# Optimization experiments

Hardware: AMD Instinct MI355X
Metric: run time of the kernel (lower is better)

Reference implementation:

```python
import jax, jax.numpy as jnp
import numpy as np

N = 50000       # num_entities / nodes
E = 100000      # edges
K = 8           # incoming edge-graph neighbors per edge
D_NODE = 64
D_EDGE = 64
H = 4
DH = D_EDGE // H
DIN = D_EDGE + 2 * D_NODE  # [edge_feat, node_feat[src], node_feat[dst]]


def setup_inputs() -> dict:
    key = jax.random.key(0)
    ks = jax.random.split(key, 6)
    node_features = jax.random.normal(ks[0], (N, D_NODE), jnp.float32)
    edge_features = jax.random.normal(ks[1], (E, D_EDGE), jnp.float32)
    edge_index = jax.random.randint(ks[2], (2, E), 0, N)
    node_tiers = jax.random.randint(ks[3], (N,), 0, 4, dtype=jnp.int32)
    # edge adjacency (line graph): each edge attends to K other edges
    adj_dst = jnp.repeat(jnp.arange(E), K)                       # [A]
    adj_src = jax.random.randint(ks[4], (E * K,), 0, E)          # [A]
    # learned params: two EdgeAttention layers, each Wq/Wk/Wv [DIN,D_EDGE], Wo [D_EDGE,D_EDGE]
    wkeys = jax.random.split(ks[5], 8)
    def w(k, fan_in, fan_out):
        return jax.random.normal(k, (fan_in, fan_out), jnp.float32) * np.float32(1.0 / np.sqrt(fan_in))
    params = {}
    for li in (1, 2):
        base = (li - 1) * 4
        params[f'l{li}_Wq'] = w(wkeys[base + 0], DIN, D_EDGE)
        params[f'l{li}_Wk'] = w(wkeys[base + 1], DIN, D_EDGE)
        params[f'l{li}_Wv'] = w(wkeys[base + 2], DIN, D_EDGE)
        params[f'l{li}_Wo'] = w(wkeys[base + 3], D_EDGE, D_EDGE)
    return dict(node_features=node_features, edge_features=edge_features,
                edge_index=edge_index, node_tiers=node_tiers,
                adj_src=adj_src, adj_dst=adj_dst, **params)


def _edge_attention(node_f, edge_f, edge_index, adj_src, adj_dst, Wq, Wk, Wv, Wo):
    # x: edge feature conditioned on endpoint node features  [E, DIN]
    x = jnp.concatenate([edge_f, node_f[edge_index[0]], node_f[edge_index[1]]], axis=-1)
    q = (x @ Wq).reshape(E, H, DH)
    k = (x @ Wk).reshape(E, H, DH)
    v = (x @ Wv).reshape(E, H, DH)
    scale = np.float32(1.0 / np.sqrt(DH))
    # scores per adjacency pair  [A, H]
    s = jnp.einsum('ahd,ahd->ah', q[adj_dst], k[adj_src]) * scale
    # segment softmax over incoming neighbors of each dst edge
    m = jax.ops.segment_max(s, adj_dst, num_segments=E)          # [E, H]
    e = jnp.exp(s - m[adj_dst])                                   # [A, H]
    denom = jax.ops.segment_sum(e, adj_dst, num_segments=E)      # [E, H]
    alpha = e / denom[adj_dst]                                    # [A, H]
    out = jax.ops.segment_sum(alpha[..., None] * v[adj_src], adj_dst, num_segments=E)  # [E,H,DH]
    return edge_f + out.reshape(E, D_EDGE) @ Wo                   # residual


def reference(node_features, edge_features, edge_index, node_tiers, adj_src, adj_dst,
              l1_Wq, l1_Wk, l1_Wv, l1_Wo, l2_Wq, l2_Wk, l2_Wv, l2_Wo):
    ef = _edge_attention(node_features, edge_features, edge_index, adj_src, adj_dst,
                         l1_Wq, l1_Wk, l1_Wv, l1_Wo)
    ef = _edge_attention(node_features, ef, edge_index, adj_src, adj_dst,
                         l2_Wq, l2_Wk, l2_Wv, l2_Wo)
    return ef  # updated edge features of the output DeltaGraph
```

## Files before the change

kernel.cpp:

```cpp
#include <hip/hip_runtime.h>

#define NE 100000
#define NN 50000

typedef short short8 __attribute__((ext_vector_type(8)));
typedef float f32x4 __attribute__((ext_vector_type(4)));
typedef unsigned short ushort;
typedef unsigned int uint;

__device__ inline ushort f2bf(float f) {
    unsigned int u = __float_as_uint(f);
    u += 0x7FFFu + ((u >> 16) & 1u);
    return (ushort)(u >> 16);
}
__device__ inline float bf2f(ushort u) {
    return __uint_as_float((unsigned int)u << 16);
}

__device__ inline short8 pack_bf8(float4 a, float4 b) {
    short8 r;
    r[0] = (short)f2bf(a.x); r[1] = (short)f2bf(a.y);
    r[2] = (short)f2bf(a.z); r[3] = (short)f2bf(a.w);
    r[4] = (short)f2bf(b.x); r[5] = (short)f2bf(b.y);
    r[6] = (short)f2bf(b.z); r[7] = (short)f2bf(b.w);
    return r;
}

__device__ inline void pack_qkv_slot(int slot, const float* Wq, const float* Wk,
                                     const float* Wv, ushort* wf)
{
    int lane = slot & 63;
    int st = slot >> 6;
    int s = st / 12, t = st % 12;
    int n = t * 16 + (lane & 15);
    int kb = s * 32 + (lane >> 4) * 8;
    const float* w = (n < 64) ? Wq : (n < 128) ? Wk : Wv;
    int nn = n & 63;
    #pragma unroll
    for (int j = 0; j < 8; ++j)
        wf[(size_t)slot * 8 + j] = f2bf(w[(size_t)(kb + j) * 64 + nn]);
}

__device__ inline void pack_wo_slot(int slot, const float* Wo, ushort* wf)
{
    int lane = slot & 63;
    int st = slot >> 6;
    int s = st / 4, t = st % 4;
    int n = t * 16 + (lane & 15);
    int kb = s * 32 + (lane >> 4) * 8;
    #pragma unroll
    for (int j = 0; j < 8; ++j)
        wf[(size_t)slot * 8 + j] = f2bf(Wo[(size_t)(kb + j) * 64 + n]);
}

__global__ __launch_bounds__(256) void prep_all(
    const float* __restrict__ l1Wq, const float* __restrict__ l1Wk,
    const float* __restrict__ l1Wv, const float* __restrict__ l1Wo,
    const float* __restrict__ l2Wq, const float* __restrict__ l2Wk,
    const float* __restrict__ l2Wv, const float* __restrict__ l2Wo,
    ushort* __restrict__ wf1, ushort* __restrict__ wf2,
    ushort* __restrict__ wo1, ushort* __restrict__ wo2)
{
    int idx = blockIdx.x * 256 + threadIdx.x;
    if (idx < 4608)            pack_qkv_slot(idx,         l1Wq, l1Wk, l1Wv, wf1);
    else if (idx < 9216)       pack_qkv_slot(idx - 4608,  l2Wq, l2Wk, l2Wv, wf2);
    else if (idx < 9728)       pack_wo_slot (idx - 9216,  l1Wo, wo1);
    else if (idx < 10240)      pack_wo_slot (idx - 9728,  l2Wo, wo2);
}

#define MFMA_B16(a, b, c) c = __builtin_amdgcn_mfma_f32_16x16x32_bf16(a, b, c, 0, 0, 0)

#define GLP const __attribute__((address_space(1))) uint*
#define LDP __attribute__((address_space(3))) uint*

#define STAGE(ph) do {                                                         \
    const char* gs_ = (const char*)wfrag + (size_t)(ph) * 24576 + (size_t)l * 16; \
    __builtin_amdgcn_global_load_lds((GLP)(gs_ + (size_t)(w*6+0)*1024), (LDP)(ldsb + (size_t)(w*6+0)*1024), 16, 0, 0); \
    __builtin_amdgcn_global_load_lds((GLP)(gs_ + (size_t)(w*6+1)*1024), (LDP)(ldsb + (size_t)(w*6+1)*1024), 16, 0, 0); \
    __builtin_amdgcn_global_load_lds((GLP)(gs_ + (size_t)(w*6+2)*1024), (LDP)(ldsb + (size_t)(w*6+2)*1024), 16, 0, 0); \
    __builtin_amdgcn_global_load_lds((GLP)(gs_ + (size_t)(w*6+3)*1024), (LDP)(ldsb + (size_t)(w*6+3)*1024), 16, 0, 0); \
    __builtin_amdgcn_global_load_lds((GLP)(gs_ + (size_t)(w*6+4)*1024), (LDP)(ldsb + (size_t)(w*6+4)*1024), 16, 0, 0); \
    __builtin_amdgcn_global_load_lds((GLP)(gs_ + (size_t)(w*6+5)*1024), (LDP)(ldsb + (size_t)(w*6+5)*1024), 16, 0, 0); \
} while (0)

#define KSTEP(Areg, si) do {                                                   \
    const char* lb_ = ldsb + (size_t)(si) * 12288 + (size_t)l * 16;            \
    short8 b0_  = *(const short8*)(lb_ + 0);                                   \
    short8 b1_  = *(const short8*)(lb_ + 1024);                                \
    short8 b2_  = *(const short8*)(lb_ + 2048);                                \
    short8 b3_  = *(const short8*)(lb_ + 3072);                                \
    short8 b4_  = *(const short8*)(lb_ + 4096);                                \
    short8 b5_  = *(const short8*)(lb_ + 5120);                                \
    short8 b6_  = *(const short8*)(lb_ + 6144);                                \
    short8 b7_  = *(const short8*)(lb_ + 7168);                                \
    short8 b8_  = *(const short8*)(lb_ + 8192);                                \
    short8 b9_  = *(const short8*)(lb_ + 9216);                                \
    short8 b10_ = *(const short8*)(lb_ + 10240);                               \
    short8 b11_ = *(const short8*)(lb_ + 11264);                               \
    MFMA_B16(Areg, b0_,  c0);  MFMA_B16(Areg, b1_,  c1);                       \
    MFMA_B16(Areg, b2_,  c2);  MFMA_B16(Areg, b3_,  c3);                       \
    MFMA_B16(Areg, b4_,  c4);  MFMA_B16(Areg, b5_,  c5);                       \
    MFMA_B16(Areg, b6_,  c6);  MFMA_B16(Areg, b7_,  c7);                       \
    MFMA_B16(Areg, b8_,  c8);  MFMA_B16(Areg, b9_,  c9);                       \
    MFMA_B16(Areg, b10_, c10); MFMA_B16(Areg, b11_, c11);                      \
} while (0)

#define STORE_T(creg, dstp, cloc) do {                                         \
    ushort* dp_ = (dstp) + (cloc);                                             \
    int row_ = e0 + kg * 4;                                                    \
    if (row_ + 0 < NE) dp_[(size_t)(row_ + 0) * 64] = f2bf(creg[0]);           \
    if (row_ + 1 < NE) dp_[(size_t)(row_ + 1) * 64] = f2bf(creg[1]);           \
    if (row_ + 2 < NE) dp_[(size_t)(row_ + 2) * 64] = f2bf(creg[2]);           \
    if (row_ + 3 < NE) dp_[(size_t)(row_ + 3) * 64] = f2bf(creg[3]);           \
} while (0)

__global__ __launch_bounds__(256) void qkv_mfma(
    const float* __restrict__ ef, const float* __restrict__ nodef,
    const int* __restrict__ eidx, const ushort* __restrict__ wfrag,
    ushort* __restrict__ qo, ushort* __restrict__ ko, ushort* __restrict__ vo)
{
    __shared__ __align__(1024) char ldsb[24 * 1024];

    const int tid = threadIdx.x;
    const int l   = tid & 63;
    const int w   = tid >> 6;
    const int r   = l & 15;
    const int kg  = l >> 4;
    const int e0  = blockIdx.x * 64 + w * 16;
    const int e   = e0 + r;
    const int ec  = (e < NE) ? e : NE - 1;

    STAGE(0);

    const int koff = kg * 8;
    const float* rp0 = ef    + (size_t)ec * 64;
    const float* rp1 = nodef + (size_t)eidx[ec] * 64;
    const float* rp2 = nodef + (size_t)eidx[NE + ec] * 64;

    short8 A0 = pack_bf8(*(const float4*)(rp0 + koff),      *(const float4*)(rp0 + koff + 4));
    short8 A1 = pack_bf8(*(const float4*)(rp0 + 32 + koff), *(const float4*)(rp0 + 36 + koff));
    short8 A2 = pack_bf8(*(const float4*)(rp1 + koff),      *(const float4*)(rp1 + koff + 4));
    short8 A3 = pack_bf8(*(const float4*)(rp1 + 32 + koff), *(const float4*)(rp1 + 36 + koff));
    short8 A4 = pack_bf8(*(const float4*)(rp2 + koff),      *(const float4*)(rp2 + koff + 4));
    short8 A5 = pack_bf8(*(const float4*)(rp2 + 32 + koff), *(const float4*)(rp2 + 36 + koff));

    f32x4 c0 = (f32x4)(0.f), c1 = (f32x4)(0.f), c2  = (f32x4)(0.f), c3  = (f32x4)(0.f);
    f32x4 c4 = (f32x4)(0.f), c5 = (f32x4)(0.f), c6  = (f32x4)(0.f), c7  = (f32x4)(0.f);
    f32x4 c8 = (f32x4)(0.f), c9 = (f32x4)(0.f), c10 = (f32x4)(0.f), c11 = (f32x4)(0.f);

    __syncthreads();
    KSTEP(A0, 0);
    KSTEP(A1, 1);
    __syncthreads();
    STAGE(1);
    __syncthreads();
    KSTEP(A2, 0);
    KSTEP(A3, 1);
    __syncthreads();
    STAGE(2);
    __syncthreads();
    KSTEP(A4, 0);
    KSTEP(A5, 1);

    STORE_T(c0,  qo, 0 * 16 + r);
    STORE_T(c1,  qo, 1 * 16 + r);
    STORE_T(c2,  qo, 2 * 16 + r);
    STORE_T(c3,  qo, 3 * 16 + r);
    STORE_T(c4,  ko, 0 * 16 + r);
    STORE_T(c5,  ko, 1 * 16 + r);
    STORE_T(c6,  ko, 2 * 16 + r);
    STORE_T(c7,  ko, 3 * 16 + r);
    STORE_T(c8,  vo, 0 * 16 + r);
    STORE_T(c9,  vo, 1 * 16 + r);
    STORE_T(c10, vo, 2 * 16 + r);
    STORE_T(c11, vo, 3 * 16 + r);
}

__global__ __launch_bounds__(256) void attn_kernel(
    const ushort* __restrict__ q, const ushort* __restrict__ kbuf,
    const ushort* __restrict__ vbuf, const int* __restrict__ adj_src,
    ushort* __restrict__ ao)
{
    const int wid  = (blockIdx.x * 256 + threadIdx.x) >> 6;
    const int lane = threadIdx.x & 63;
    if (wid >= NE) return;
    const int e    = wid;
    const int half = lane >> 5;
    const int l32  = lane & 31;

    const int4 nb = *(const int4*)(adj_src + e * 8 + half * 4);
    const int nbr0 = nb.x, nbr1 = nb.y, nbr2 = nb.z, nbr3 = nb.w;

    ushort2 qu = *(const ushort2*)(q + (size_t)e * 64 + l32 * 2);
    const float q0 = bf2f(qu.x), q1 = bf2f(qu.y);

    ushort2 ku0 = *(const ushort2*)(kbuf + (size_t)nbr0 * 64 + l32 * 2);
    ushort2 ku1 = *(const ushort2*)(kbuf + (size_t)nbr1 * 64 + l32 * 2);
    ushort2 ku2 = *(const ushort2*)(kbuf + (size_t)nbr2 * 64 + l32 * 2);
    ushort2 ku3 = *(const ushort2*)(kbuf + (size_t)nbr3 * 64 + l32 * 2);
    ushort2 vu0 = *(const ushort2*)(vbuf + (size_t)nbr0 * 64 + l32 * 2);
    ushort2 vu1 = *(const ushort2*)(vbuf + (size_t)nbr1 * 64 + l32 * 2);
    ushort2 vu2 = *(const ushort2*)(vbuf + (size_t)nbr2 * 64 + l32 * 2);
    ushort2 vu3 = *(const ushort2*)(vbuf + (size_t)nbr3 * 64 + l32 * 2);

    float s0 = q0 * bf2f(ku0.x) + q1 * bf2f(ku0.y);
    float s1 = q0 * bf2f(ku1.x) + q1 * bf2f(ku1.y);
    float s2 = q0 * bf2f(ku2.x) + q1 * bf2f(ku2.y);
    float s3 = q0 * bf2f(ku3.x) + q1 * bf2f(ku3.y);
    s0 += __shfl_xor(s0, 1); s0 += __shfl_xor(s0, 2); s0 += __shfl_xor(s0, 4);
    s1 += __shfl_xor(s1, 1); s1 += __shfl_xor(s1, 2); s1 += __shfl_xor(s1, 4);
    s2 += __shfl_xor(s2, 1); s2 += __shfl_xor(s2, 2); s2 += __shfl_xor(s2, 4);
    s3 += __shfl_xor(s3, 1); s3 += __shfl_xor(s3, 2); s3 += __shfl_xor(s3, 4);
    s0 *= 0.25f; s1 *= 0.25f; s2 *= 0.25f; s3 *= 0.25f;

    float m = fmaxf(fmaxf(s0, s1), fmaxf(s2, s3));
    m = fmaxf(m, __shfl_xor(m, 32));
    float w0 = __expf(s0 - m), w1 = __expf(s1 - m);
    float w2 = __expf(s2 - m), w3 = __expf(s3 - m);
    float den = w0 + w1 + w2 + w3;
    den += __shfl_xor(den, 32);
    const float inv = 1.f / den;

    float ox = 0.f, oy = 0.f;
    ox = fmaf(w0, bf2f(vu0.x), ox); oy = fmaf(w0, bf2f(vu0.y), oy);
    ox = fmaf(w1, bf2f(vu1.x), ox); oy = fmaf(w1, bf2f(vu1.y), oy);
    ox = fmaf(w2, bf2f(vu2.x), ox); oy = fmaf(w2, bf2f(vu2.y), oy);
    ox = fmaf(w3, bf2f(vu3.x), ox); oy = fmaf(w3, bf2f(vu3.y), oy);
    ox = (ox + __shfl_xor(ox, 32)) * inv;
    oy = (oy + __shfl_xor(oy, 32)) * inv;

    if (lane < 32) {
        ushort2 o;
        o.x = f2bf(ox);
        o.y = f2bf(oy);
        *(ushort2*)(ao + (size_t)e * 64 + l32 * 2) = o;
    }
}

__global__ __launch_bounds__(256) void wo_mfma(
    const float* __restrict__ ef_in, const ushort* __restrict__ attn,
    const ushort* __restrict__ wofrag, float* __restrict__ efo)
{
    const int wave = threadIdx.x >> 6;
    const int lane = threadIdx.x & 63;
    const int r  = lane & 15;
    const int kg = lane >> 4;
    const int e0 = blockIdx.x * 64 + wave * 16;
    const int e  = e0 + r;
    const int ec = (e < NE) ? e : NE - 1;

    short8 af0 = *(const short8*)(attn + (size_t)ec * 64 + kg * 8);
    short8 af1 = *(const short8*)(attn + (size_t)ec * 64 + 32 + kg * 8);

    const char* wf = (const char*)wofrag + (size_t)lane * 16;
    f32x4 d0 = (f32x4)(0.f), d1 = (f32x4)(0.f), d2 = (f32x4)(0.f), d3 = (f32x4)(0.f);
    short8 g0 = *(const short8*)(wf + 0 * 1024);
    short8 g1 = *(const short8*)(wf + 1 * 1024);
    short8 g2 = *(const short8*)(wf + 2 * 1024);
    short8 g3 = *(const short8*)(wf + 3 * 1024);
    MFMA_B16(af0, g0, d0); MFMA_B16(af0, g1, d1);
    MFMA_B16(af0, g2, d2); MFMA_B16(af0, g3, d3);
    g0 = *(const short8*)(wf + 4 * 1024);
    g1 = *(const short8*)(wf + 5 * 1024);
    g2 = *(const short8*)(wf + 6 * 1024);
    g3 = *(const short8*)(wf + 7 * 1024);
    MFMA_B16(af1, g0, d0); MFMA_B16(af1, g1, d1);
    MFMA_B16(af1, g2, d2); MFMA_B16(af1, g3, d3);

    const int orow = e0 + kg * 4;
    #pragma unroll
    for (int t = 0; t < 4; ++t) {
        const f32x4 dd = (t == 0) ? d0 : (t == 1) ? d1 : (t == 2) ? d2 : d3;
        const int c = t * 16 + r;
        #pragma unroll
        for (int j = 0; j < 4; ++j) {
            int row = orow + j;
            if (row < NE) {
                size_t off = (size_t)row * 64 + c;
                efo[off] = dd[j] + ef_in[off];
            }
        }
    }
}

extern "C" void kernel_launch(void* const* d_in, const int* in_sizes, int n_in,
                              void* d_out, int out_size, void* d_ws, size_t ws_size,
                              hipStream_t stream)
{
    const float* nodef   = (const float*)d_in[0];
    const float* ef      = (const float*)d_in[1];
    const int*   eidx    = (const int*)d_in[2];
    const int*   adj_src = (const int*)d_in[4];
    const float* l1Wq = (const float*)d_in[6];
    const float* l1Wk = (const float*)d_in[7];
    const float* l1Wv = (const float*)d_in[8];
    const float* l1Wo = (const float*)d_in[9];
    const float* l2Wq = (const float*)d_in[10];
    const float* l2Wk = (const float*)d_in[11];
    const float* l2Wv = (const float*)d_in[12];
    const float* l2Wo = (const float*)d_in[13];

    ushort* q  = (ushort*)d_ws;
    ushort* k  = q  + (size_t)NE * 64;
    ushort* v  = k  + (size_t)NE * 64;
    ushort* ao = v  + (size_t)NE * 64;
    ushort* wf1 = ao + (size_t)NE * 64;
    ushort* wf2 = wf1 + 36864;
    ushort* wo1 = wf2 + 36864;
    ushort* wo2 = wo1 + 4096;
    float* out = (float*)d_out;

    dim3 blk(256);
    const int gq = (NE + 63) / 64;
    const int ga = (NE + 3) / 4;
    const int gw = (NE + 63) / 64;

    prep_all<<<40, blk, 0, stream>>>(l1Wq, l1Wk, l1Wv, l1Wo,
                                     l2Wq, l2Wk, l2Wv, l2Wo,
                                     wf1, wf2, wo1, wo2);

    qkv_mfma<<<gq, blk, 0, stream>>>(ef, nodef, eidx, wf1, q, k, v);
    attn_kernel<<<ga, blk, 0, stream>>>(q, k, v, adj_src, ao);
    wo_mfma<<<gw, blk, 0, stream>>>(ef, ao, wo1, out);
    qkv_mfma<<<gq, blk, 0, stream>>>(out, nodef, eidx, wf2, q, k, v);
    attn_kernel<<<ga, blk, 0, stream>>>(q, k, v, adj_src, ao);
    wo_mfma<<<gw, blk, 0, stream>>>(out, ao, wo2, out);
}
```

Measured before the change: 149.2 us.

## Restructure QKV GEMM: per-wave output-column split, direct B loads, LDS-staged coalesced stores

The QKV projection kernel now gives each block 32 edges. Each wave computes 3 of the 12 output column tiles for both 16-row groups, reading weight fragments straight from global/L2 instead of staging all weights into LDS with barriers between phases. Results are transposed through a small LDS buffer and written as coalesced 16-byte rows for q, k and v, replacing the scattered 2-byte strided stores. The trade is more redundant A-row gathers per edge across waves and more weight traffic per block, in exchange for no phase barriers, smaller LDS, and much better store coalescing.

```diff
diff --git a/kernel.cpp b/kernel.cpp
--- a/kernel.cpp
+++ b/kernel.cpp
@@ -70,110 +70,95 @@
 
 #define MFMA_B16(a, b, c) c = __builtin_amdgcn_mfma_f32_16x16x32_bf16(a, b, c, 0, 0, 0)
 
-#define GLP const __attribute__((address_space(1))) uint*
-#define LDP __attribute__((address_space(3))) uint*
-
-#define STAGE(ph) do {                                                         \
-    const char* gs_ = (const char*)wfrag + (size_t)(ph) * 24576 + (size_t)l * 16; \
-    __builtin_amdgcn_global_load_lds((GLP)(gs_ + (size_t)(w*6+0)*1024), (LDP)(ldsb + (size_t)(w*6+0)*1024), 16, 0, 0); \
-    __builtin_amdgcn_global_load_lds((GLP)(gs_ + (size_t)(w*6+1)*1024), (LDP)(ldsb + (size_t)(w*6+1)*1024), 16, 0, 0); \
-    __builtin_amdgcn_global_load_lds((GLP)(gs_ + (size_t)(w*6+2)*1024), (LDP)(ldsb + (size_t)(w*6+2)*1024), 16, 0, 0); \
-    __builtin_amdgcn_global_load_lds((GLP)(gs_ + (size_t)(w*6+3)*1024), (LDP)(ldsb + (size_t)(w*6+3)*1024), 16, 0, 0); \
-    __builtin_amdgcn_global_load_lds((GLP)(gs_ + (size_t)(w*6+4)*1024), (LDP)(ldsb + (size_t)(w*6+4)*1024), 16, 0, 0); \
-    __builtin_amdgcn_global_load_lds((GLP)(gs_ + (size_t)(w*6+5)*1024), (LDP)(ldsb + (size_t)(w*6+5)*1024), 16, 0, 0); \
+#define LOADROW(pref, ptr) \
+    float4 pref##_0 = *(const float4*)((ptr) + koff);        \
+    float4 pref##_1 = *(const float4*)((ptr) + koff + 4);    \
+    float4 pref##_2 = *(const float4*)((ptr) + 32 + koff);   \
+    float4 pref##_3 = *(const float4*)((ptr) + 32 + koff + 4);
+
+#define LOADB(s) \
+    short8 B##s##_0 = *(const short8*)(wfb + (size_t)((s) * 12 + 3 * w) * 1024);        \
+    short8 B##s##_1 = *(const short8*)(wfb + (size_t)((s) * 12 + 3 * w) * 1024 + 1024); \
+    short8 B##s##_2 = *(const short8*)(wfb + (size_t)((s) * 12 + 3 * w) * 1024 + 2048);
+
+#define MSTEP(s) \
+    MFMA_B16(A0s##s, B##s##_0, d00); MFMA_B16(A0s##s, B##s##_1, d01); \
+    MFMA_B16(A0s##s, B##s##_2, d02);                                  \
+    MFMA_B16(A1s##s, B##s##_0, d10); MFMA_B16(A1s##s, B##s##_1, d11); \
+    MFMA_B16(A1s##s, B##s##_2, d12);
+
+#define DUMPB(dreg, T_lit, n_lit) do {                                         \
+    ushort* p_ = ldso + ((T_lit) * 16 + kg * 4) * 200 + (3 * w + (n_lit)) * 16 + r; \
+    p_[0]   = f2bf(dreg[0]); p_[200] = f2bf(dreg[1]);                          \
+    p_[400] = f2bf(dreg[2]); p_[600] = f2bf(dreg[3]);                          \
 } while (0)
 
-#define KSTEP(Areg, si) do {                                                   \
-    const char* lb_ = ldsb + (size_t)(si) * 12288 + (size_t)l * 16;            \
-    short8 b0_  = *(const short8*)(lb_ + 0);                                   \
-    short8 b1_  = *(const short8*)(lb_ + 1024);                                \
-    short8 b2_  = *(const short8*)(lb_ + 2048);                                \
-    short8 b3_  = *(const short8*)(lb_ + 3072);                                \
-    short8 b4_  = *(const short8*)(lb_ + 4096);                                \
-    short8 b5_  = *(const short8*)(lb_ + 5120);                                \
-    short8 b6_  = *(const short8*)(lb_ + 6144);                                \
-    short8 b7_  = *(const short8*)(lb_ + 7168);                                \
-    short8 b8_  = *(const short8*)(lb_ + 8192);                                \
-    short8 b9_  = *(const short8*)(lb_ + 9216);                                \
-    short8 b10_ = *(const short8*)(lb_ + 10240);                               \
-    short8 b11_ = *(const short8*)(lb_ + 11264);                               \
-    MFMA_B16(Areg, b0_,  c0);  MFMA_B16(Areg, b1_,  c1);                       \
-    MFMA_B16(Areg, b2_,  c2);  MFMA_B16(Areg, b3_,  c3);                       \
-    MFMA_B16(Areg, b4_,  c4);  MFMA_B16(Areg, b5_,  c5);                       \
-    MFMA_B16(Areg, b6_,  c6);  MFMA_B16(Areg, b7_,  c7);                       \
-    MFMA_B16(Areg, b8_,  c8);  MFMA_B16(Areg, b9_,  c9);                       \
-    MFMA_B16(Areg, b10_, c10); MFMA_B16(Areg, b11_, c11);                      \
-} while (0)
-
-#define STORE_T(creg, dstp, cloc) do {                                         \
-    ushort* dp_ = (dstp) + (cloc);                                             \
-    int row_ = e0 + kg * 4;                                                    \
-    if (row_ + 0 < NE) dp_[(size_t)(row_ + 0) * 64] = f2bf(creg[0]);           \
-    if (row_ + 1 < NE) dp_[(size_t)(row_ + 1) * 64] = f2bf(creg[1]);           \
-    if (row_ + 2 < NE) dp_[(size_t)(row_ + 2) * 64] = f2bf(creg[2]);           \
-    if (row_ + 3 < NE) dp_[(size_t)(row_ + 3) * 64] = f2bf(creg[3]);           \
-} while (0)
-
-__global__ __launch_bounds__(256) void qkv_mfma(
+__global__ __launch_bounds__(256, 2) void qkv_mfma(
     const float* __restrict__ ef, const float* __restrict__ nodef,
     const int* __restrict__ eidx, const ushort* __restrict__ wfrag,
     ushort* __restrict__ qo, ushort* __restrict__ ko, ushort* __restrict__ vo)
 {
-    __shared__ __align__(1024) char ldsb[24 * 1024];
+    __shared__ __align__(16) ushort ldso[32 * 200];
 
     const int tid = threadIdx.x;
     const int l   = tid & 63;
     const int w   = tid >> 6;
     const int r   = l & 15;
     const int kg  = l >> 4;
-    const int e0  = blockIdx.x * 64 + w * 16;
-    const int e   = e0 + r;
-    const int ec  = (e < NE) ? e : NE - 1;
-
-    STAGE(0);
-
+    const int e0  = blockIdx.x * 32;
+
+    const int ea  = e0 + r;
+    const int eb  = e0 + 16 + r;
+    const int eac = (ea < NE) ? ea : NE - 1;
+    const int ebc = (eb < NE) ? eb : NE - 1;
     const int koff = kg * 8;
-    const float* rp0 = ef    + (size_t)ec * 64;
-    const float* rp1 = nodef + (size_t)eidx[ec] * 64;
-    const float* rp2 = nodef + (size_t)eidx[NE + ec] * 64;
-
-    short8 A0 = pack_bf8(*(const float4*)(rp0 + koff),      *(const float4*)(rp0 + koff + 4));
-    short8 A1 = pack_bf8(*(const float4*)(rp0 + 32 + koff), *(const float4*)(rp0 + 36 + koff));
-    short8 A2 = pack_bf8(*(const float4*)(rp1 + koff),      *(const float4*)(rp1 + koff + 4));
-    short8 A3 = pack_bf8(*(const float4*)(rp1 + 32 + koff), *(const float4*)(rp1 + 36 + koff));
-    short8 A4 = pack_bf8(*(const float4*)(rp2 + koff),      *(const float4*)(rp2 + koff + 4));
-    short8 A5 = pack_bf8(*(const float4*)(rp2 + 32 + koff), *(const float4*)(rp2 + 36 + koff));
-
-    f32x4 c0 = (f32x4)(0.f), c1 = (f32x4)(0.f), c2  = (f32x4)(0.f), c3  = (f32x4)(0.f);
-    f32x4 c4 = (f32x4)(0.f), c5 = (f32x4)(0.f), c6  = (f32x4)(0.f), c7  = (f32x4)(0.f);
-    f32x4 c8 = (f32x4)(0.f), c9 = (f32x4)(0.f), c10 = (f32x4)(0.f), c11 = (f32x4)(0.f);
-
+
+    const int sa = eidx[eac];
+    const int da = eidx[NE + eac];
+    const int sb = eidx[ebc];
+    const int db = eidx[NE + ebc];
+
+    LOADROW(xa0, ef    + (size_t)eac * 64)
+    LOADROW(xa1, nodef + (size_t)sa  * 64)
+    LOADROW(xa2, nodef + (size_t)da  * 64)
+    LOADROW(xb0, ef    + (size_t)ebc * 64)
+    LOADROW(xb1, nodef + (size_t)sb  * 64)
+    LOADROW(xb2, nodef + (size_t)db  * 64)
+
+    const char* wfb = (const char*)wfrag + (size_t)l * 16;
+    LOADB(0) LOADB(1) LOADB(2) LOADB(3) LOADB(4) LOADB(5)
+
+    short8 A0s0 = pack_bf8(xa0_0, xa0_1);
+    short8 A0s1 = pack_bf8(xa0_2, xa0_3);
+    short8 A0s2 = pack_bf8(xa1_0, xa1_1);
+    short8 A0s3 = pack_bf8(xa1_2, xa1_3);
+    short8 A0s4 = pack_bf8(xa2_0, xa2_1);
+    short8 A0s5 = pack_bf8(xa2_2, xa2_3);
+    short8 A1s0 = pack_bf8(xb0_0, xb0_1);
+    short8 A1s1 = pack_bf8(xb0_2, xb0_3);
+    short8 A1s2 = pack_bf8(xb1_0, xb1_1);
+    short8 A1s3 = pack_bf8(xb1_2, xb1_3);
+    short8 A1s4 = pack_bf8(xb2_0, xb2_1);
+    short8 A1s5 = pack_bf8(xb2_2, xb2_3);
+
+    f32x4 d00 = (f32x4)(0.f), d01 = (f32x4)(0.f), d02 = (f32x4)(0.f);
+    f32x4 d10 = (f32x4)(0.f), d11 = (f32x4)(0.f), d12 = (f32x4)(0.f);
+
+    MSTEP(0) MSTEP(1) MSTEP(2) MSTEP(3) MSTEP(4) MSTEP(5)
+
+    DUMPB(d00, 0, 0); DUMPB(d01, 0, 1); DUMPB(d02, 0, 2);
+    DUMPB(d10, 1, 0); DUMPB(d11, 1, 1); DUMPB(d12, 1, 2);
     __syncthreads();
-    KSTEP(A0, 0);
-    KSTEP(A1, 1);
-    __syncthreads();
-    STAGE(1);
-    __syncthreads();
-    KSTEP(A2, 0);
-    KSTEP(A3, 1);
-    __syncthreads();
-    STAGE(2);
-    __syncthreads();
-    KSTEP(A4, 0);
-    KSTEP(A5, 1);
-
-    STORE_T(c0,  qo, 0 * 16 + r);
-    STORE_T(c1,  qo, 1 * 16 + r);
-    STORE_T(c2,  qo, 2 * 16 + r);
-    STORE_T(c3,  qo, 3 * 16 + r);
-    STORE_T(c4,  ko, 0 * 16 + r);
-    STORE_T(c5,  ko, 1 * 16 + r);
-    STORE_T(c6,  ko, 2 * 16 + r);
-    STORE_T(c7,  ko, 3 * 16 + r);
-    STORE_T(c8,  vo, 0 * 16 + r);
-    STORE_T(c9,  vo, 1 * 16 + r);
-    STORE_T(c10, vo, 2 * 16 + r);
-    STORE_T(c11, vo, 3 * 16 + r);
+
+    const int row  = tid >> 3;
+    const int seg  = tid & 7;
+    const int grow = e0 + row;
+    if (grow < NE) {
+        const ushort* rp = ldso + row * 200;
+        *(short8*)(qo + (size_t)grow * 64 + seg * 8) = *(const short8*)(rp +   0 + seg * 8);
+        *(short8*)(ko + (size_t)grow * 64 + seg * 8) = *(const short8*)(rp +  64 + seg * 8);
+        *(short8*)(vo + (size_t)grow * 64 + seg * 8) = *(const short8*)(rp + 128 + seg * 8);
+    }
 }
 
 __global__ __launch_bounds__(256) void attn_kernel(
@@ -300,18 +285,18 @@
     const float* l2Wv = (const float*)d_in[12];
     const float* l2Wo = (const float*)d_in[13];
 
-    ushort* q  = (ushort*)d_ws;
-    ushort* k  = q  + (size_t)NE * 64;
-    ushort* v  = k  + (size_t)NE * 64;
-    ushort* ao = v  + (size_t)NE * 64;
-    ushort* wf1 = ao + (size_t)NE * 64;
+    ushort* q   = (ushort*)d_ws;
+    ushort* k   = q   + (size_t)NE * 64;
+    ushort* v   = k   + (size_t)NE * 64;
+    ushort* ao  = v   + (size_t)NE * 64;
+    ushort* wf1 = ao  + (size_t)NE * 64;
     ushort* wf2 = wf1 + 36864;
     ushort* wo1 = wf2 + 36864;
     ushort* wo2 = wo1 + 4096;
     float* out = (float*)d_out;
 
     dim3 blk(256);
-    const int gq = (NE + 63) / 64;
+    const int gq = (NE + 31) / 32;
     const int ga = (NE + 3) / 4;
     const int gw = (NE + 63) / 64;
 
```

Result: slower. 185.8 us (+24.5%).
